# Kernel tuning notes

Measured on AMD Instinct MI355X. Metric: run time of the kernel, lower is better.

The kernel has to match this reference:

```python
import jax, jax.numpy as jnp
import numpy as np

B, T, D, H, L = 32, 2048, 256, 256, 2  # batch, seq, input, hidden, layers


def setup_inputs() -> dict:
    key = jax.random.key(0)
    k = jax.random.split(key, 5)
    s = 1.0 / np.sqrt(H)  # torch default uniform(-1/sqrt(H), 1/sqrt(H))
    return {
        "x": jax.random.normal(k[0], (B, T, D), jnp.float32),
        "Wih": jax.random.uniform(k[1], (L, 3 * H, D), jnp.float32, -s, s),
        "Whh": jax.random.uniform(k[2], (L, 3 * H, H), jnp.float32, -s, s),
        "bih": jax.random.uniform(k[3], (L, 3 * H), jnp.float32, -s, s),
        "bhh": jax.random.uniform(k[4], (L, 3 * H), jnp.float32, -s, s),
    }


def _gru_layer(x, Wih, Whh, bih, bhh):
    # x: [B, T, Din] -> [B, T, H]; gate order (r, z, n) as in nn.GRUCell
    xg = jnp.einsum('btd,gd->btg', x, Wih) + bih  # precompute input gates [B,T,3H]

    def step(h, xg_t):
        hg = h @ Whh.T + bhh                      # [B, 3H]
        xr, xz, xn = jnp.split(xg_t, 3, axis=-1)
        hr, hz, hn = jnp.split(hg, 3, axis=-1)
        r = jax.nn.sigmoid(xr + hr)
        z = jax.nn.sigmoid(xz + hz)
        n = jnp.tanh(xn + r * hn)
        h_new = (1.0 - z) * n + z * h
        return h_new, h_new

    h0 = jnp.zeros((x.shape[0], Whh.shape[1]), x.dtype)
    _, hs = jax.lax.scan(step, h0, jnp.swapaxes(xg, 0, 1))  # [T, B, H]
    return jnp.swapaxes(hs, 0, 1)


def reference(x, Wih, Whh, bih, bhh):
    # batch_first stacked unidirectional GRU; returns last layer's sequence [B, T, H]
    h = x
    for l in range(Wih.shape[0]):
        h = _gru_layer(h, Wih[l], Whh[l], bih[l], bhh[l])
    return h
```

## Files before the change

### kernel.cpp

```cpp
#include <hip/hip_runtime.h>

typedef _Float16 half_t;
typedef _Float16 half2_t __attribute__((ext_vector_type(2)));
typedef unsigned int       u32;
typedef unsigned short     u16;

#define BB    32
#define TT    2048
#define HH    256
#define G3    768
#define CHUNK 8
#define NBUF  4
#define NSLOT (CHUNK * NBUF)
#define NCK   (TT / CHUNK)

#define OFF_CONS 12288
#define OFF_XG0  24576
#define OFF_XG1  3170304
#define OFF_H0   6316032
#define FLAGS_BYTES 24576

__device__ __forceinline__ half2_t f2h2(float a, float b) {
  half2_t r; r.x = (half_t)a; r.y = (half_t)b; return r;
}
__device__ __forceinline__ float sigm(float v) {
  return __builtin_amdgcn_rcpf(1.f + __builtin_amdgcn_exp2f(v * -1.4426950408889634f));
}
__device__ __forceinline__ float tanh_fast(float v) {
  return 1.f - 2.f * __builtin_amdgcn_rcpf(1.f + __builtin_amdgcn_exp2f(v * 2.8853900817779268f));
}
__device__ __forceinline__ void wait_ge(u32* p, u32 v) {
  u32 x = __hip_atomic_load(p, __ATOMIC_ACQUIRE, __HIP_MEMORY_SCOPE_AGENT);
  while (x < v) {
    __builtin_amdgcn_s_sleep(1);
    x = __hip_atomic_load(p, __ATOMIC_RELAXED, __HIP_MEMORY_SCOPE_AGENT);
    if (x >= v)
      x = __hip_atomic_load(p, __ATOMIC_ACQUIRE, __HIP_MEMORY_SCOPE_AGENT);
  }
  asm volatile("" :: "v"(x));
}
__device__ __forceinline__ float ld_f32_agent(const float* p) {
  return __hip_atomic_load(p, __ATOMIC_RELAXED, __HIP_MEMORY_SCOPE_AGENT);
}
__device__ __forceinline__ u32 ld_u32_agent(const u32* p) {
  return __hip_atomic_load(p, __ATOMIC_RELAXED, __HIP_MEMORY_SCOPE_AGENT);
}
__device__ __forceinline__ void st_f32_agent(float* p, float v) {
  __hip_atomic_store(p, v, __ATOMIC_RELAXED, __HIP_MEMORY_SCOPE_AGENT);
}
__device__ __forceinline__ void st_u16_agent(u16* p, u16 v) {
  __hip_atomic_store(p, v, __ATOMIC_RELAXED, __HIP_MEMORY_SCOPE_AGENT);
}
__device__ __forceinline__ void barrier_lds() {
  asm volatile("s_waitcnt lgkmcnt(0)" ::: "memory");
  __builtin_amdgcn_s_barrier();
  asm volatile("" ::: "memory");
}

__device__ __forceinline__ void dot3(const half2_t* hrow, const u32 (&w)[3][64],
                                     float& a0, float& a1, float& a2) {
  const float4* hv4 = (const float4*)hrow;
#pragma unroll
  for (int j4 = 0; j4 < 16; ++j4) {
    float4 q = hv4[j4];
    half2_t hh[4];
    hh[0] = __builtin_bit_cast(half2_t, q.x);
    hh[1] = __builtin_bit_cast(half2_t, q.y);
    hh[2] = __builtin_bit_cast(half2_t, q.z);
    hh[3] = __builtin_bit_cast(half2_t, q.w);
#pragma unroll
    for (int u = 0; u < 4; ++u) {
      const int idx = j4 * 4 + u;
      a0 = __builtin_amdgcn_fdot2(__builtin_bit_cast(half2_t, w[0][idx]), hh[u], a0, false);
      a1 = __builtin_amdgcn_fdot2(__builtin_bit_cast(half2_t, w[1][idx]), hh[u], a1, false);
      a2 = __builtin_amdgcn_fdot2(__builtin_bit_cast(half2_t, w[2][idx]), hh[u], a2, false);
    }
  }
}

__global__ __launch_bounds__(512) __attribute__((amdgpu_waves_per_eu(2, 2)))
void gru_pipe(const float* __restrict__ x,
              const float* __restrict__ Wih,
              const float* __restrict__ Whh,
              const float* __restrict__ bih,
              const float* __restrict__ bhh,
              float* __restrict__ out,
              uint8_t* __restrict__ ws)
{
  const int stage = blockIdx.x >> 5;
  const int chain = blockIdx.x & 31;
  const int tid   = threadIdx.x;
  const int i     = (tid >> 6) * 32 + (tid & 31);
  const int c     = (tid >> 5) & 1;
  const int l     = stage >> 1;
  const bool rec  = (stage & 1);

  u32*    flags = (u32*)ws;
  u32*    cons  = (u32*)(ws + OFF_CONS);
  float*  xg0q  = (float*)(ws + OFF_XG0);
  float*  xg1q  = (float*)(ws + OFF_XG1);
  half_t* h0q   = (half_t*)(ws + OFF_H0);

  const float* Wm = (rec ? Whh : Wih) + (size_t)l * G3 * HH;
  const float* bv = (rec ? bhh : bih) + (size_t)l * G3;

  u32   w[3][64];
  float bs[3];
#pragma unroll
  for (int r = 0; r < 3; ++r) {
    const int row = r * 256 + i;
    const float4* wp = (const float4*)(Wm + (size_t)row * HH + c * 128);
#pragma unroll
    for (int j = 0; j < 32; ++j) {
      float4 v = wp[j];
      w[r][2 * j]     = __builtin_bit_cast(u32, f2h2(v.x, v.y));
      w[r][2 * j + 1] = __builtin_bit_cast(u32, f2h2(v.z, v.w));
    }
    bs[r] = bv[row];
  }
#pragma unroll
  for (int r = 0; r < 3; ++r)
#pragma unroll
    for (int j = 0; j < 64; ++j)
      asm volatile("" : "+v"(w[r][j]));

  __shared__ __align__(16) half2_t hb4[CHUNK][128];
  if (tid < 128) {
    half2_t z; z.x = (half_t)0.f; z.y = (half_t)0.f;
#pragma unroll
    for (int s = 0; s < CHUNK; ++s) hb4[s][tid] = z;
  }

  float   hprev = 0.f;
  half2_t xreg[CHUNK];
  if (stage == 0 && tid < 128) {
#pragma unroll
    for (int s = 0; s < CHUNK; ++s) {
      float2 v = ((const float2*)(x + (size_t)(chain * TT + s) * HH))[tid];
      xreg[s] = f2h2(v.x, v.y);
    }
  }

  float* xgq_in  = (stage == 1) ? xg0q : xg1q;
  float* xgq_out = (stage == 0) ? xg0q : xg1q;
  u32* flag_in   = flags + ((size_t)((stage - 1) * BB + chain)) * 32;
  u32* flag_out  = flags + ((size_t)(stage * BB + chain)) * 32;
  u32* cons_in   = cons + ((size_t)((stage - 1) * BB + chain)) * 32;
  u32* cons_out  = cons + ((size_t)(stage * BB + chain)) * 32;

  __syncthreads();

  for (int ck = 0; ck < NCK; ++ck) {
    const int g = ck & (NBUF - 1);
    const size_t qs = (size_t)chain * NSLOT + g * CHUNK;

    if (stage > 0 && tid == 0)                     wait_ge(flag_in + g, (u32)(ck + 1));
    if (stage < 3 && ck >= NBUF && tid == 256)     wait_ge(cons_out, (u32)(ck - NBUF + 1));
    __syncthreads();

    if (tid == 0 && ck > 0) {
      if (stage < 3)
        __hip_atomic_store(flag_out + ((ck - 1) & (NBUF - 1)), (u32)ck,
                           __ATOMIC_RELEASE, __HIP_MEMORY_SCOPE_AGENT);
      if (rec)
        __hip_atomic_store(cons_in, (u32)ck,
                           __ATOMIC_RELAXED, __HIP_MEMORY_SCOPE_AGENT);
    }

    if (!rec) {
      if (stage == 0) {
        if (tid < 128) {
#pragma unroll
          for (int s = 0; s < CHUNK; ++s) hb4[s][tid] = xreg[s];
        }
      } else {
        if (tid < 128) {
#pragma unroll
          for (int s = 0; s < CHUNK; ++s) {
            u32 v = ld_u32_agent((const u32*)(h0q + (qs + s) * HH) + tid);
            hb4[s][tid] = __builtin_bit_cast(half2_t, v);
          }
        }
      }
      barrier_lds();
      if (stage == 2 && tid == 0)
        __hip_atomic_store(cons_in, (u32)(ck + 1),
                           __ATOMIC_RELAXED, __HIP_MEMORY_SCOPE_AGENT);
      if (stage == 0 && tid < 128 && ck + 1 < NCK) {
#pragma unroll
        for (int s = 0; s < CHUNK; ++s) {
          float2 v = ((const float2*)(x + (size_t)(chain * TT + (ck + 1) * CHUNK + s) * HH))[tid];
          xreg[s] = f2h2(v.x, v.y);
        }
      }
#pragma unroll
      for (int s = 0; s < CHUNK; ++s) {
        float a0 = 0.f, a1 = 0.f, a2 = 0.f;
        dot3(&hb4[s][c * 64], w, a0, a1, a2);
        a0 += __shfl_xor(a0, 32, 64);
        a1 += __shfl_xor(a1, 32, 64);
        a2 += __shfl_xor(a2, 32, 64);
        if (c == 0) {
          float* qo = xgq_out + (qs + s) * G3;
          st_f32_agent(qo + i,       a0 + bs[0]);
          st_f32_agent(qo + 256 + i, a1 + bs[1]);
          st_f32_agent(qo + 512 + i, a2 + bs[2]);
        }
      }
    } else {
      const float* q0 = xgq_in + qs * G3;
      float xr_a = 0.f, xz_a = 0.f, xn_a = 0.f;
      float xr_b = 0.f, xz_b = 0.f, xn_b = 0.f;
      if (c == 0) {
        xr_a = ld_f32_agent(q0 + i);
        xz_a = ld_f32_agent(q0 + 256 + i);
        xn_a = ld_f32_agent(q0 + 512 + i);
        xr_b = ld_f32_agent(q0 + G3 + i);
        xz_b = ld_f32_agent(q0 + G3 + 256 + i);
        xn_b = ld_f32_agent(q0 + G3 + 512 + i);
      }
#pragma unroll
      for (int s = 0; s < CHUNK; ++s) {
        float xr_c = 0.f, xz_c = 0.f, xn_c = 0.f;
        if (c == 0 && s + 2 < CHUNK) {
          const float* qn = q0 + (s + 2) * G3;
          xr_c = ld_f32_agent(qn + i);
          xz_c = ld_f32_agent(qn + 256 + i);
          xn_c = ld_f32_agent(qn + 512 + i);
        }
        float a0 = 0.f, a1 = 0.f, a2 = 0.f;
        dot3(&hb4[s & 1][c * 64], w, a0, a1, a2);
        a0 += __shfl_xor(a0, 32, 64);
        a1 += __shfl_xor(a1, 32, 64);
        a2 += __shfl_xor(a2, 32, 64);
        if (c == 0) {
          float r    = sigm(xr_a + a0 + bs[0]);
          float z    = sigm(xz_a + a1 + bs[1]);
          float n    = tanh_fast(xn_a + r * (a2 + bs[2]));
          float hnew = n + z * (hprev - n);
          hprev = hnew;
          ((half_t*)&hb4[(s + 1) & 1][0])[i] = (half_t)hnew;
          if (stage == 1) {
            half_t hv = (half_t)hnew;
            st_u16_agent((u16*)(h0q + (qs + s) * HH + i),
                         __builtin_bit_cast(u16, hv));
          } else {
            out[(size_t)(chain * TT + ck * CHUNK + s) * HH + i] = hnew;
          }
          xr_a = xr_b; xz_a = xz_b; xn_a = xn_b;
          xr_b = xr_c; xz_b = xz_c; xn_b = xn_c;
        }
        if (s < CHUNK - 1) barrier_lds();
      }
    }
  }

  __syncthreads();
  if (tid == 0 && stage < 3)
    __hip_atomic_store(flag_out + ((NCK - 1) & (NBUF - 1)), (u32)NCK,
                       __ATOMIC_RELEASE, __HIP_MEMORY_SCOPE_AGENT);
}

extern "C" void kernel_launch(void* const* d_in, const int* in_sizes, int n_in,
                              void* d_out, int out_size, void* d_ws, size_t ws_size,
                              hipStream_t stream) {
  hipMemsetAsync(d_ws, 0, FLAGS_BYTES, stream);
  hipLaunchKernelGGL(gru_pipe, dim3(128), dim3(512), 0, stream,
                     (const float*)d_in[0], (const float*)d_in[1], (const float*)d_in[2],
                     (const float*)d_in[3], (const float*)d_in[4],
                     (float*)d_out, (uint8_t*)d_ws);
}
```

Baseline: 2.801 ms.

## Use MFMA 16x16x32 f16 for recurrent matvec in GRU recurrent stages

The recurrent stages now compute the h·Whh^T matvec with MFMA 16x16x32 f16 instructions instead of per-thread fdot2 loops followed by cross-half shuffles. Weights are held in registers in MFMA B-fragment layout, and the A operand is the broadcast hidden state read from LDS. Only column 0 of each accumulator is used, so most MFMA output is wasted, but the goal is to shorten the serial per-step latency. The kernel is also split into separate input-projection and recurrent code paths, and the xg prefetch depth drops from two steps to one.

```diff
diff --git a/kernel.cpp b/kernel.cpp
--- a/kernel.cpp
+++ b/kernel.cpp
@@ -2,7 +2,10 @@
 
 typedef _Float16 half_t;
 typedef _Float16 half2_t __attribute__((ext_vector_type(2)));
+typedef _Float16 half8_t __attribute__((ext_vector_type(8)));
+typedef float    f32x4   __attribute__((ext_vector_type(4)));
 typedef unsigned int       u32;
+typedef u32      u32x4   __attribute__((ext_vector_type(4)));
 typedef unsigned short     u16;
 
 #define BB    32
@@ -90,8 +93,6 @@
   const int stage = blockIdx.x >> 5;
   const int chain = blockIdx.x & 31;
   const int tid   = threadIdx.x;
-  const int i     = (tid >> 6) * 32 + (tid & 31);
-  const int c     = (tid >> 5) & 1;
   const int l     = stage >> 1;
   const bool rec  = (stage & 1);
 
@@ -104,41 +105,11 @@
   const float* Wm = (rec ? Whh : Wih) + (size_t)l * G3 * HH;
   const float* bv = (rec ? bhh : bih) + (size_t)l * G3;
 
-  u32   w[3][64];
-  float bs[3];
-#pragma unroll
-  for (int r = 0; r < 3; ++r) {
-    const int row = r * 256 + i;
-    const float4* wp = (const float4*)(Wm + (size_t)row * HH + c * 128);
-#pragma unroll
-    for (int j = 0; j < 32; ++j) {
-      float4 v = wp[j];
-      w[r][2 * j]     = __builtin_bit_cast(u32, f2h2(v.x, v.y));
-      w[r][2 * j + 1] = __builtin_bit_cast(u32, f2h2(v.z, v.w));
-    }
-    bs[r] = bv[row];
-  }
-#pragma unroll
-  for (int r = 0; r < 3; ++r)
-#pragma unroll
-    for (int j = 0; j < 64; ++j)
-      asm volatile("" : "+v"(w[r][j]));
-
   __shared__ __align__(16) half2_t hb4[CHUNK][128];
   if (tid < 128) {
     half2_t z; z.x = (half_t)0.f; z.y = (half_t)0.f;
 #pragma unroll
     for (int s = 0; s < CHUNK; ++s) hb4[s][tid] = z;
-  }
-
-  float   hprev = 0.f;
-  half2_t xreg[CHUNK];
-  if (stage == 0 && tid < 128) {
-#pragma unroll
-    for (int s = 0; s < CHUNK; ++s) {
-      float2 v = ((const float2*)(x + (size_t)(chain * TT + s) * HH))[tid];
-      xreg[s] = f2h2(v.x, v.y);
-    }
   }
 
   float* xgq_in  = (stage == 1) ? xg0q : xg1q;
@@ -148,26 +119,51 @@
   u32* cons_in   = cons + ((size_t)((stage - 1) * BB + chain)) * 32;
   u32* cons_out  = cons + ((size_t)(stage * BB + chain)) * 32;
 
-  __syncthreads();
-
-  for (int ck = 0; ck < NCK; ++ck) {
-    const int g = ck & (NBUF - 1);
-    const size_t qs = (size_t)chain * NSLOT + g * CHUNK;
-
-    if (stage > 0 && tid == 0)                     wait_ge(flag_in + g, (u32)(ck + 1));
-    if (stage < 3 && ck >= NBUF && tid == 256)     wait_ge(cons_out, (u32)(ck - NBUF + 1));
+  if (!rec) {
+    const int i = (tid >> 6) * 32 + (tid & 31);
+    const int c = (tid >> 5) & 1;
+    u32   w[3][64];
+    float bs[3];
+#pragma unroll
+    for (int r = 0; r < 3; ++r) {
+      const int row = r * 256 + i;
+      const float4* wp = (const float4*)(Wm + (size_t)row * HH + c * 128);
+#pragma unroll
+      for (int j = 0; j < 32; ++j) {
+        float4 v = wp[j];
+        w[r][2 * j]     = __builtin_bit_cast(u32, f2h2(v.x, v.y));
+        w[r][2 * j + 1] = __builtin_bit_cast(u32, f2h2(v.z, v.w));
+      }
+      bs[r] = bv[row];
+    }
+#pragma unroll
+    for (int r = 0; r < 3; ++r)
+#pragma unroll
+      for (int j = 0; j < 64; ++j)
+        asm volatile("" : "+v"(w[r][j]));
+
+    half2_t xreg[CHUNK];
+    if (stage == 0 && tid < 128) {
+#pragma unroll
+      for (int s = 0; s < CHUNK; ++s) {
+        float2 v = ((const float2*)(x + (size_t)(chain * TT + s) * HH))[tid];
+        xreg[s] = f2h2(v.x, v.y);
+      }
+    }
     __syncthreads();
 
-    if (tid == 0 && ck > 0) {
-      if (stage < 3)
+    for (int ck = 0; ck < NCK; ++ck) {
+      const int g = ck & (NBUF - 1);
+      const size_t qs = (size_t)chain * NSLOT + g * CHUNK;
+
+      if (stage > 0 && tid == 0)                 wait_ge(flag_in + g, (u32)(ck + 1));
+      if (ck >= NBUF && tid == 256)              wait_ge(cons_out, (u32)(ck - NBUF + 1));
+      __syncthreads();
+
+      if (tid == 0 && ck > 0)
         __hip_atomic_store(flag_out + ((ck - 1) & (NBUF - 1)), (u32)ck,
                            __ATOMIC_RELEASE, __HIP_MEMORY_SCOPE_AGENT);
-      if (rec)
-        __hip_atomic_store(cons_in, (u32)ck,
-                           __ATOMIC_RELAXED, __HIP_MEMORY_SCOPE_AGENT);
-    }
-
-    if (!rec) {
+
       if (stage == 0) {
         if (tid < 128) {
 #pragma unroll
@@ -207,58 +203,118 @@
           st_f32_agent(qo + 512 + i, a2 + bs[2]);
         }
       }
-    } else {
+    }
+    __syncthreads();
+    if (tid == 0)
+      __hip_atomic_store(flag_out + ((NCK - 1) & (NBUF - 1)), (u32)NCK,
+                         __ATOMIC_RELEASE, __HIP_MEMORY_SCOPE_AGENT);
+  } else {
+    const int wv = tid >> 6;
+    const int lane = tid & 63;
+    const int lr = lane & 15;
+    const int g4 = lane >> 4;
+    const int j0 = wv * 16 + lr;
+    const bool act = (g4 < 2);
+    const int idx = g4 * 128 + j0;
+
+    u32x4 wf[6][8];
+#pragma unroll
+    for (int tt = 0; tt < 6; ++tt) {
+      const int row = tt * 128 + j0;
+#pragma unroll
+      for (int kk = 0; kk < 8; ++kk) {
+        const float4* p = (const float4*)(Wm + (size_t)row * HH + kk * 32 + g4 * 8);
+        float4 qa = p[0], qb = p[1];
+        u32x4 v;
+        v.x = __builtin_bit_cast(u32, f2h2(qa.x, qa.y));
+        v.y = __builtin_bit_cast(u32, f2h2(qa.z, qa.w));
+        v.z = __builtin_bit_cast(u32, f2h2(qb.x, qb.y));
+        v.w = __builtin_bit_cast(u32, f2h2(qb.z, qb.w));
+        wf[tt][kk] = v;
+      }
+    }
+#pragma unroll
+    for (int tt = 0; tt < 6; ++tt)
+#pragma unroll
+      for (int kk = 0; kk < 8; ++kk)
+        asm volatile("" : "+v"(wf[tt][kk]));
+
+    float bR = 0.f, bZ = 0.f, bN = 0.f;
+    if (act) { bR = bv[idx]; bZ = bv[256 + idx]; bN = bv[512 + idx]; }
+    float hprev = 0.f;
+    __syncthreads();
+
+    for (int ck = 0; ck < NCK; ++ck) {
+      const int g = ck & (NBUF - 1);
+      const size_t qs = (size_t)chain * NSLOT + g * CHUNK;
+
+      if (tid == 0)                              wait_ge(flag_in + g, (u32)(ck + 1));
+      if (stage < 3 && ck >= NBUF && tid == 256) wait_ge(cons_out, (u32)(ck - NBUF + 1));
+      __syncthreads();
+
+      if (tid == 0 && ck > 0) {
+        if (stage < 3)
+          __hip_atomic_store(flag_out + ((ck - 1) & (NBUF - 1)), (u32)ck,
+                             __ATOMIC_RELEASE, __HIP_MEMORY_SCOPE_AGENT);
+        __hip_atomic_store(cons_in, (u32)ck,
+                           __ATOMIC_RELAXED, __HIP_MEMORY_SCOPE_AGENT);
+      }
+
       const float* q0 = xgq_in + qs * G3;
-      float xr_a = 0.f, xz_a = 0.f, xn_a = 0.f;
-      float xr_b = 0.f, xz_b = 0.f, xn_b = 0.f;
-      if (c == 0) {
-        xr_a = ld_f32_agent(q0 + i);
-        xz_a = ld_f32_agent(q0 + 256 + i);
-        xn_a = ld_f32_agent(q0 + 512 + i);
-        xr_b = ld_f32_agent(q0 + G3 + i);
-        xz_b = ld_f32_agent(q0 + G3 + 256 + i);
-        xn_b = ld_f32_agent(q0 + G3 + 512 + i);
+      float xr = 0.f, xz = 0.f, xn = 0.f;
+      if (act) {
+        xr = ld_f32_agent(q0 + idx);
+        xz = ld_f32_agent(q0 + 256 + idx);
+        xn = ld_f32_agent(q0 + 512 + idx);
       }
 #pragma unroll
       for (int s = 0; s < CHUNK; ++s) {
-        float xr_c = 0.f, xz_c = 0.f, xn_c = 0.f;
-        if (c == 0 && s + 2 < CHUNK) {
-          const float* qn = q0 + (s + 2) * G3;
-          xr_c = ld_f32_agent(qn + i);
-          xz_c = ld_f32_agent(qn + 256 + i);
-          xn_c = ld_f32_agent(qn + 512 + i);
-        }
-        float a0 = 0.f, a1 = 0.f, a2 = 0.f;
-        dot3(&hb4[s & 1][c * 64], w, a0, a1, a2);
-        a0 += __shfl_xor(a0, 32, 64);
-        a1 += __shfl_xor(a1, 32, 64);
-        a2 += __shfl_xor(a2, 32, 64);
-        if (c == 0) {
-          float r    = sigm(xr_a + a0 + bs[0]);
-          float z    = sigm(xz_a + a1 + bs[1]);
-          float n    = tanh_fast(xn_a + r * (a2 + bs[2]));
+        float xrn = 0.f, xzn = 0.f, xnn = 0.f;
+        if (act && s + 1 < CHUNK) {
+          const float* qn = q0 + (s + 1) * G3;
+          xrn = ld_f32_agent(qn + idx);
+          xzn = ld_f32_agent(qn + 256 + idx);
+          xnn = ld_f32_agent(qn + 512 + idx);
+        }
+        f32x4 acc[6];
+#pragma unroll
+        for (int tt = 0; tt < 6; ++tt) acc[tt] = (f32x4){0.f, 0.f, 0.f, 0.f};
+        const float4* ab = (const float4*)((const half_t*)&hb4[s & 1][0]);
+#pragma unroll
+        for (int kk = 0; kk < 8; ++kk) {
+          half8_t af = __builtin_bit_cast(half8_t, ab[kk * 4 + g4]);
+#pragma unroll
+          for (int tt = 0; tt < 6; ++tt)
+            acc[tt] = __builtin_amdgcn_mfma_f32_16x16x32_f16(
+                af, __builtin_bit_cast(half8_t, wf[tt][kk]), acc[tt], 0, 0, 0);
+        }
+        if (act) {
+          float aR = g4 ? acc[1][0] : acc[0][0];
+          float aZ = g4 ? acc[3][0] : acc[2][0];
+          float aN = g4 ? acc[5][0] : acc[4][0];
+          float r    = sigm(xr + aR + bR);
+          float z    = sigm(xz + aZ + bZ);
+          float n    = tanh_fast(xn + r * (aN + bN));
           float hnew = n + z * (hprev - n);
           hprev = hnew;
-          ((half_t*)&hb4[(s + 1) & 1][0])[i] = (half_t)hnew;
+          ((half_t*)&hb4[(s + 1) & 1][0])[idx] = (half_t)hnew;
           if (stage == 1) {
             half_t hv = (half_t)hnew;
-            st_u16_agent((u16*)(h0q + (qs + s) * HH + i),
+            st_u16_agent((u16*)(h0q + (qs + s) * HH + idx),
                          __builtin_bit_cast(u16, hv));
           } else {
-            out[(size_t)(chain * TT + ck * CHUNK + s) * HH + i] = hnew;
+            out[(size_t)(chain * TT + ck * CHUNK + s) * HH + idx] = hnew;
           }
-          xr_a = xr_b; xz_a = xz_b; xn_a = xn_b;
-          xr_b = xr_c; xz_b = xz_c; xn_b = xn_c;
+          xr = xrn; xz = xzn; xn = xnn;
         }
         if (s < CHUNK - 1) barrier_lds();
       }
     }
+    __syncthreads();
+    if (tid == 0 && stage < 3)
+      __hip_atomic_store(flag_out + ((NCK - 1) & (NBUF - 1)), (u32)NCK,
+                         __ATOMIC_RELEASE, __HIP_MEMORY_SCOPE_AGENT);
   }
-
-  __syncthreads();
-  if (tid == 0 && stage < 3)
-    __hip_atomic_store(flag_out + ((NCK - 1) & (NBUF - 1)), (u32)NCK,
-                       __ATOMIC_RELEASE, __HIP_MEMORY_SCOPE_AGENT);
 }
 
 extern "C" void kernel_launch(void* const* d_in, const int* in_sizes, int n_in,
```

Result: no change. 2.771 ms (-1.1%).
